# Performance work log

Hardware: AMD Instinct MI355X
Metric: run time of the kernel (lower is better)

## Reference

```python
import jax, jax.numpy as jnp
import numpy as np

B, S, D = 4, 2048, 1024
R = 64
N_FQK = N_FV = N_RQK = N_RV = 32
N_HEADS = 16
D_HEAD = D // N_HEADS


def setup_inputs() -> dict:
    key = jax.random.key(0)
    ks = jax.random.split(key, 10)

    def orth_bank(k, n, rows, cols):
        # mimic per-slice orthogonal init
        a = jax.random.normal(k, (n, rows, cols), dtype=jnp.float32)
        q, _ = jnp.linalg.qr(a) if rows >= cols else (jnp.swapaxes(jnp.linalg.qr(jnp.swapaxes(a, -1, -2))[0], -1, -2), None)
        return q.astype(jnp.float32)

    return {
        "x": jax.random.normal(ks[0], (B, S, D), dtype=jnp.float32),
        "fqk_weights": jax.random.uniform(ks[1], (B, S, N_FQK), dtype=jnp.float32),
        "fv_weights": jax.random.uniform(ks[2], (B, S, N_FV), dtype=jnp.float32),
        "rqk_weights_Q": jax.random.uniform(ks[3], (B, S, N_RQK), dtype=jnp.float32),
        "rqk_weights_K": jax.random.uniform(ks[4], (B, S, N_RQK), dtype=jnp.float32),
        "rv_weights": jax.random.uniform(ks[5], (B, S, N_RV), dtype=jnp.float32),
        "f_neurons": orth_bank(ks[6], N_FQK + N_FV, D, R),   # (64, D, R)
        "r_neurons": orth_bank(ks[7], N_RQK + N_RV, R, D),   # (64, R, D)
        "W_O": jax.random.normal(ks[8], (D, D), dtype=jnp.float32) * (1.0 / np.sqrt(D)),
    }


def reference(x, fqk_weights, fv_weights, rqk_weights_Q, rqk_weights_K, rv_weights,
              f_neurons, r_neurons, W_O):
    fqk = f_neurons[:N_FQK]          # (N, D, R)
    fv = f_neurons[N_FQK:]
    rqk = r_neurons[:N_RQK]          # (N, R, D)
    rv = r_neurons[N_RQK:]

    # Fused routed low-rank projections (same math as bsn,ndr->bsdr then bsd,bsdr->bsr,
    # reassociated to avoid the (B,S,D,R) intermediate).
    h_qk = jnp.einsum('bsd,bsn,ndr->bsr', x, fqk_weights, fqk)
    h_v = jnp.einsum('bsd,bsn,ndr->bsr', x, fv_weights, fv)

    Q = jnp.einsum('bsr,bsn,nrd->bsd', h_qk, rqk_weights_Q, rqk)
    K = jnp.einsum('bsr,bsn,nrd->bsd', h_qk, rqk_weights_K, rqk)
    V = jnp.einsum('bsr,bsn,nrd->bsd', h_v, rv_weights, rv)

    def heads(t):  # (B,S,D) -> (B,H,S,Dh)
        return t.reshape(B, S, N_HEADS, D_HEAD).transpose(0, 2, 1, 3)

    Qh, Kh, Vh = heads(Q), heads(K), heads(V)
    scores = jnp.einsum('bhqd,bhkd->bhqk', Qh, Kh) / np.sqrt(D_HEAD).astype(np.float32)
    causal = jnp.triu(jnp.ones((S, S), dtype=bool), k=1)
    scores = jnp.where(causal[None, None], -jnp.inf, scores)
    attn = jax.nn.softmax(scores, axis=-1)
    attn_out = jnp.einsum('bhqk,bhkd->bhqd', attn, Vh)
    attn_out = attn_out.transpose(0, 2, 1, 3).reshape(B, S, D)
    return attn_out @ W_O.T
```

## Files before the change

### kernel.cpp

```cpp
#include <hip/hip_runtime.h>
#include <hip/hip_bf16.h>


namespace {
constexpr int kS = 2048;
constexpr int kD = 1024;
}

typedef unsigned short u16;
typedef __attribute__((ext_vector_type(4))) float f32x4;
typedef __attribute__((ext_vector_type(8))) short s8v;

union FragU { s8v s; unsigned u[4]; };

__device__ __forceinline__ u16 f2bf_bits(float f) {
  union { float f; unsigned u; } cv; cv.f = f;
  unsigned u = cv.u;
  unsigned r = u + 0x7fffu + ((u >> 16) & 1u);
  return (u16)(r >> 16);
}
__device__ __forceinline__ float bf2f(u16 b) {
  union { unsigned u; float f; } cv; cv.u = ((unsigned)b) << 16; return cv.f;
}
__device__ __forceinline__ unsigned pk_bf16(float a, float b) {
  __hip_bfloat162 h = __float22bfloat162_rn(make_float2(a, b));
  union { __hip_bfloat162 h; unsigned u; } cv; cv.h = h; return cv.u;
}

__global__ __launch_bounds__(256) void t1_kernel(const float* __restrict__ f,
                                                 u16* __restrict__ FT) {
  __shared__ float Tt[64 * 132];
  const int tid = threadIdx.x;
  const int d0 = blockIdx.x * 128;
  const int n  = blockIdx.y;
#pragma unroll
  for (int e = 0; e < 8; ++e) {
    int flat = tid + e * 256;
    int dd = flat >> 4, r4 = (flat & 15) * 4;
    float4 v = *(const float4*)&f[((size_t)n * kD + d0 + dd) * 64 + r4];
    Tt[(r4 + 0) * 132 + dd] = v.x;
    Tt[(r4 + 1) * 132 + dd] = v.y;
    Tt[(r4 + 2) * 132 + dd] = v.z;
    Tt[(r4 + 3) * 132 + dd] = v.w;
  }
  __syncthreads();
#pragma unroll
  for (int e = 0; e < 4; ++e) {
    int flat = tid + e * 256;
    int r = flat >> 4, dq = (flat & 15) * 8;
    const float* p = &Tt[r * 132 + dq];
    uint4 o = { pk_bf16(p[0], p[1]), pk_bf16(p[2], p[3]),
                pk_bf16(p[4], p[5]), pk_bf16(p[6], p[7]) };
    *(uint4*)&FT[((size_t)n * 64 + r) * kD + d0 + dq] = o;
  }
}

__global__ __launch_bounds__(256) void t2_kernel(const float* __restrict__ rn,
                                                 u16* __restrict__ RT) {
  __shared__ float Tt[128 * 68];
  const int tid = threadIdx.x;
  const int d0 = blockIdx.x * 128;
  const int n  = blockIdx.y;
#pragma unroll
  for (int e = 0; e < 8; ++e) {
    int flat = tid + e * 256;
    int r = flat >> 5, d4 = (flat & 31) * 4;
    float4 v = *(const float4*)&rn[((size_t)n * 64 + r) * kD + d0 + d4];
    Tt[(d4 + 0) * 68 + r] = v.x;
    Tt[(d4 + 1) * 68 + r] = v.y;
    Tt[(d4 + 2) * 68 + r] = v.z;
    Tt[(d4 + 3) * 68 + r] = v.w;
  }
  __syncthreads();
#pragma unroll
  for (int e = 0; e < 4; ++e) {
    int flat = tid + e * 256;
    int dd = flat >> 3, rq = (flat & 7) * 8;
    const float* p = &Tt[dd * 68 + rq];
    uint4 o = { pk_bf16(p[0], p[1]), pk_bf16(p[2], p[3]),
                pk_bf16(p[4], p[5]), pk_bf16(p[6], p[7]) };
    *(uint4*)&RT[((size_t)(d0 + dd)) * 4096 + n * 64 + rq] = o;
  }
}

__global__ __launch_bounds__(256) void g_gemm(const float* __restrict__ x,
                                              const u16* __restrict__ FT,
                                              u16* __restrict__ G) {
  __shared__ short As[128 * 72];
  __shared__ short Bs[128 * 72];
  const int tid = threadIdx.x;
  const int lane = tid & 63, wid = tid >> 6;
  const int wm = wid & 1, wn = wid >> 1;
  const int quad = lane >> 4, l15 = lane & 15;
  const int cT = blockIdx.x * 128;
  const int tok0 = blockIdx.y * 128;

  f32x4 acc[4][4];
#pragma unroll
  for (int mt = 0; mt < 4; ++mt)
#pragma unroll
    for (int nt = 0; nt < 4; ++nt) acc[mt][nt] = {0.f, 0.f, 0.f, 0.f};

#pragma unroll 1
  for (int d0 = 0; d0 < kD; d0 += 64) {
    __syncthreads();
#pragma unroll
    for (int e = 0; e < 8; ++e) {
      int flat = tid + e * 256;
      int row = flat >> 4, kq = (flat & 15) * 4;
      float4 v = *(const float4*)&x[(size_t)(tok0 + row) * kD + d0 + kq];
      uint2 o = { pk_bf16(v.x, v.y), pk_bf16(v.z, v.w) };
      *(uint2*)&As[row * 72 + kq] = o;
    }
#pragma unroll
    for (int e = 0; e < 4; ++e) {
      int flat = tid + e * 256;
      int col = flat >> 3, kq = (flat & 7) * 8;
      *(s8v*)&Bs[col * 72 + kq] =
          *(const s8v*)&FT[(size_t)(cT + col) * kD + d0 + kq];
    }
    __syncthreads();
    s8v a0[4], a1[4], b0[4], b1[4];
#pragma unroll
    for (int mt = 0; mt < 4; ++mt) {
      const short* p = &As[(wm * 64 + mt * 16 + l15) * 72 + quad * 8];
      a0[mt] = *(const s8v*)p;
      a1[mt] = *(const s8v*)(p + 32);
    }
#pragma unroll
    for (int nt = 0; nt < 4; ++nt) {
      const short* p = &Bs[(wn * 64 + nt * 16 + l15) * 72 + quad * 8];
      b0[nt] = *(const s8v*)p;
      b1[nt] = *(const s8v*)(p + 32);
    }
#pragma unroll
    for (int mt = 0; mt < 4; ++mt)
#pragma unroll
      for (int nt = 0; nt < 4; ++nt) {
        acc[mt][nt] = __builtin_amdgcn_mfma_f32_16x16x32_bf16(
            a0[mt], b0[nt], acc[mt][nt], 0, 0, 0);
        acc[mt][nt] = __builtin_amdgcn_mfma_f32_16x16x32_bf16(
            a1[mt], b1[nt], acc[mt][nt], 0, 0, 0);
      }
  }
#pragma unroll
  for (int mt = 0; mt < 4; ++mt)
#pragma unroll
    for (int nt = 0; nt < 4; ++nt) {
      int col = cT + wn * 64 + nt * 16 + l15;
      int rbase = tok0 + wm * 64 + mt * 16 + quad * 4;
#pragma unroll
      for (int i = 0; i < 4; ++i)
        G[(size_t)(rbase + i) * 4096 + col] = f2bf_bits(acc[mt][nt][i]);
    }
}

__global__ __launch_bounds__(256) void reduce_h(const u16* __restrict__ G,
                                                const float* __restrict__ fqk_w,
                                                const float* __restrict__ fv_w,
                                                float* __restrict__ h_qk,
                                                float* __restrict__ h_v) {
  int idx = blockIdx.x * 256 + threadIdx.x;
  int t = idx >> 4, r4 = (idx & 15) * 4;
  float4 aq = {0.f, 0.f, 0.f, 0.f}, av = {0.f, 0.f, 0.f, 0.f};
  const u16* gq = &G[(size_t)t * 4096 + r4];
  const u16* gv = gq + 2048;
#pragma unroll 4
  for (int n = 0; n < 32; ++n) {
    float wa = fqk_w[t * 32 + n];
    float wb = fv_w[t * 32 + n];
    ushort4 g1 = *(const ushort4*)&gq[n * 64];
    ushort4 g2 = *(const ushort4*)&gv[n * 64];
    aq.x += wa * bf2f(g1.x); aq.y += wa * bf2f(g1.y);
    aq.z += wa * bf2f(g1.z); aq.w += wa * bf2f(g1.w);
    av.x += wb * bf2f(g2.x); av.y += wb * bf2f(g2.y);
    av.z += wb * bf2f(g2.z); av.w += wb * bf2f(g2.w);
  }
  *(float4*)&h_qk[t * 64 + r4] = aq;
  *(float4*)&h_v[t * 64 + r4] = av;
}

__global__ __launch_bounds__(256) void qkv_gemm(
    const float* __restrict__ h_qk, const float* __restrict__ h_v,
    const float* __restrict__ wq, const float* __restrict__ wk,
    const float* __restrict__ wv, const u16* __restrict__ RT,
    u16* __restrict__ Qb, u16* __restrict__ Kb, u16* __restrict__ VTg) {
  __shared__ float hs[128 * 68];
  __shared__ float wsl[128 * 33];
  short* Bs = (short*)hs;
  const int tid = threadIdx.x;
  const int lane = tid & 63, wid = tid >> 6;
  const int wm = wid & 1, wn = wid >> 1;
  const int quad = lane >> 4, l15 = lane & 15;
  const int dT = blockIdx.x * 128;
  const int tok0 = blockIdx.y * 128;
  const int which = blockIdx.z;
  const float* __restrict__ h = (which == 2) ? h_v : h_qk;
  const float* __restrict__ w = (which == 0) ? wq : (which == 1) ? wk : wv;
  const int g0 = (which == 2) ? 2048 : 0;

#pragma unroll
  for (int e = 0; e < 8; ++e) {
    int flat = tid + e * 256;
    int row = flat >> 4, rq = (flat & 15) * 4;
    *(float4*)&hs[row * 68 + rq] =
        *(const float4*)&h[(size_t)(tok0 + row) * 64 + rq];
  }
#pragma unroll
  for (int e = 0; e < 16; ++e) {
    int flat = tid + e * 256;
    int row = flat >> 5, nn = flat & 31;
    wsl[row * 33 + nn] = w[(size_t)(tok0 + row) * 32 + nn];
  }
  __syncthreads();

  f32x4 hreg[4][4];
#pragma unroll
  for (int mt = 0; mt < 4; ++mt) {
    const float* hp = &hs[(wm * 64 + mt * 16 + l15) * 68 + quad * 8];
    hreg[mt][0] = *(const f32x4*)hp;
    hreg[mt][1] = *(const f32x4*)(hp + 4);
    hreg[mt][2] = *(const f32x4*)(hp + 32);
    hreg[mt][3] = *(const f32x4*)(hp + 36);
  }

  f32x4 acc[4][4];
#pragma unroll
  for (int mt = 0; mt < 4; ++mt)
#pragma unroll
    for (int nt = 0; nt < 4; ++nt) acc[mt][nt] = {0.f, 0.f, 0.f, 0.f};

#pragma unroll 1
  for (int n = 0; n < 32; ++n) {
    __syncthreads();
#pragma unroll
    for (int e = 0; e < 4; ++e) {
      int flat = tid + e * 256;
      int col = flat >> 3, kq = (flat & 7) * 8;
      *(s8v*)&Bs[col * 72 + kq] =
          *(const s8v*)&RT[(size_t)(dT + col) * 4096 + g0 + n * 64 + kq];
    }
    __syncthreads();
    s8v a0[4], a1[4], b0[4], b1[4];
#pragma unroll
    for (int mt = 0; mt < 4; ++mt) {
      float wv_ = wsl[(wm * 64 + mt * 16 + l15) * 33 + n];
      FragU fa, fb;
      fa.u[0] = pk_bf16(wv_ * hreg[mt][0][0], wv_ * hreg[mt][0][1]);
      fa.u[1] = pk_bf16(wv_ * hreg[mt][0][2], wv_ * hreg[mt][0][3]);
      fa.u[2] = pk_bf16(wv_ * hreg[mt][1][0], wv_ * hreg[mt][1][1]);
      fa.u[3] = pk_bf16(wv_ * hreg[mt][1][2], wv_ * hreg[mt][1][3]);
      a0[mt] = fa.s;
      fb.u[0] = pk_bf16(wv_ * hreg[mt][2][0], wv_ * hreg[mt][2][1]);
      fb.u[1] = pk_bf16(wv_ * hreg[mt][2][2], wv_ * hreg[mt][2][3]);
      fb.u[2] = pk_bf16(wv_ * hreg[mt][3][0], wv_ * hreg[mt][3][1]);
      fb.u[3] = pk_bf16(wv_ * hreg[mt][3][2], wv_ * hreg[mt][3][3]);
      a1[mt] = fb.s;
    }
#pragma unroll
    for (int nt = 0; nt < 4; ++nt) {
      const short* p = &Bs[(wn * 64 + nt * 16 + l15) * 72 + quad * 8];
      b0[nt] = *(const s8v*)p;
      b1[nt] = *(const s8v*)(p + 32);
    }
#pragma unroll
    for (int mt = 0; mt < 4; ++mt)
#pragma unroll
      for (int nt = 0; nt < 4; ++nt) {
        acc[mt][nt] = __builtin_amdgcn_mfma_f32_16x16x32_bf16(
            a0[mt], b0[nt], acc[mt][nt], 0, 0, 0);
        acc[mt][nt] = __builtin_amdgcn_mfma_f32_16x16x32_bf16(
            a1[mt], b1[nt], acc[mt][nt], 0, 0, 0);
      }
  }

  if (which < 2) {
    u16* __restrict__ O = (which == 0) ? Qb : Kb;
#pragma unroll
    for (int mt = 0; mt < 4; ++mt)
#pragma unroll
      for (int nt = 0; nt < 4; ++nt) {
        int col = dT + wn * 64 + nt * 16 + l15;
        int rbase = tok0 + wm * 64 + mt * 16 + quad * 4;
#pragma unroll
        for (int i = 0; i < 4; ++i)
          O[(size_t)(rbase + i) * kD + col] = f2bf_bits(acc[mt][nt][i]);
      }
  } else {
#pragma unroll
    for (int mt = 0; mt < 4; ++mt)
#pragma unroll
      for (int nt = 0; nt < 4; ++nt) {
        int d = dT + wn * 64 + nt * 16 + l15;
        int hh = d >> 6, dl = d & 63;
        int t = tok0 + wm * 64 + mt * 16 + quad * 4;
        int bb = t >> 11, sl = t & 2047;
        ushort4 u = { f2bf_bits(acc[mt][nt][0]), f2bf_bits(acc[mt][nt][1]),
                      f2bf_bits(acc[mt][nt][2]), f2bf_bits(acc[mt][nt][3]) };
        *(ushort4*)&VTg[(((size_t)bb * 16 + hh) * 64 + dl) * kS + sl] = u;
      }
  }
}

__global__ __launch_bounds__(512) void attn_mfma(
    const u16* __restrict__ Qb, const u16* __restrict__ Kb,
    const u16* __restrict__ VTg, u16* __restrict__ AOb)
{
  __shared__ short Qs[128 * 72];
  __shared__ short Ks[64 * 72];
  __shared__ short VTs[64 * 72];
  __shared__ short Ps[8][16 * 72];
  const int tid = threadIdx.x;
  const int lane = tid & 63, w = tid >> 6;
  const int quad = lane >> 4, l15 = lane & 15;
  const int qb = 15 - blockIdx.x;
  const int hh = blockIdx.y, b = blockIdx.z;
  const int dh = hh * 64;
  const size_t qrow0 = (size_t)b * kS + (size_t)qb * 128;
  const int ktmax = qb * 2 + 1;
  const u16* __restrict__ vbase = VTg + ((size_t)(b * 16 + hh) * 64) * kS;

  const int prow = tid >> 3;
  const int pd8  = (tid & 7) * 8;

  *(uint4*)&Qs[prow * 72 + pd8] =
      *(const uint4*)&Qb[(qrow0 + prow) * kD + dh + pd8];
  *(uint4*)&Qs[(prow + 64) * 72 + pd8] =
      *(const uint4*)&Qb[(qrow0 + prow + 64) * kD + dh + pd8];
  *(uint4*)&Ks[prow * 72 + pd8] =
      *(const uint4*)&Kb[((size_t)b * kS + prow) * kD + dh + pd8];
  *(uint4*)&VTs[prow * 72 + pd8] =
      *(const uint4*)&vbase[(size_t)prow * kS + pd8];
  __syncthreads();

  s8v bq0 = *(const s8v*)&Qs[(w * 16 + l15) * 72 + quad * 8];
  s8v bq1 = *(const s8v*)&Qs[(w * 16 + l15) * 72 + 32 + quad * 8];

  const int q_g = qb * 128 + w * 16 + l15;
  const int qmax_w = qb * 128 + w * 16 + 15;
  float m = -INFINITY, l = 0.f;
  f32x4 O[4];
#pragma unroll
  for (int dt = 0; dt < 4; ++dt) O[dt] = {0.f, 0.f, 0.f, 0.f};

#pragma unroll 1
  for (int kt = 0; kt <= ktmax; ++kt) {
    uint4 pk, pv;
    if (kt < ktmax) {
      const size_t krn = (size_t)b * kS + (size_t)(kt + 1) * 64;
      pk = *(const uint4*)&Kb[(krn + prow) * kD + dh + pd8];
      pv = *(const uint4*)&vbase[(size_t)prow * kS + (kt + 1) * 64 + pd8];
    }

    if (kt * 64 <= qmax_w) {
      f32x4 st[4];
#pragma unroll
      for (int nt = 0; nt < 4; ++nt) {
        const short* p = &Ks[(nt * 16 + l15) * 72 + quad * 8];
        s8v ak0 = *(const s8v*)p;
        s8v ak1 = *(const s8v*)(p + 32);
        f32x4 z = {0.f, 0.f, 0.f, 0.f};
        z = __builtin_amdgcn_mfma_f32_16x16x32_bf16(ak0, bq0, z, 0, 0, 0);
        st[nt] = __builtin_amdgcn_mfma_f32_16x16x32_bf16(ak1, bq1, z, 0, 0, 0);
      }

      if (kt * 64 + 63 > qb * 128 + w * 16) {
#pragma unroll
        for (int nt = 0; nt < 4; ++nt)
#pragma unroll
          for (int i = 0; i < 4; ++i)
            if (kt * 64 + nt * 16 + quad * 4 + i > q_g) st[nt][i] = -1e30f;
      }

      float pm = -INFINITY;
#pragma unroll
      for (int nt = 0; nt < 4; ++nt)
#pragma unroll
        for (int i = 0; i < 4; ++i) pm = fmaxf(pm, st[nt][i]);
      pm = fmaxf(pm, __shfl_xor(pm, 16, 64));
      pm = fmaxf(pm, __shfl_xor(pm, 32, 64));
      float mn = fmaxf(m, pm);
      float alpha = __expf((m - mn) * 0.125f);
      m = mn;
      float p[4][4];
      float r = 0.f;
#pragma unroll
      for (int nt = 0; nt < 4; ++nt)
#pragma unroll
        for (int i = 0; i < 4; ++i) {
          p[nt][i] = __expf((st[nt][i] - mn) * 0.125f);
          r += p[nt][i];
        }
      r += __shfl_xor(r, 16, 64);
      r += __shfl_xor(r, 32, 64);
      l = l * alpha + r;
#pragma unroll
      for (int dt = 0; dt < 4; ++dt)
#pragma unroll
        for (int i = 0; i < 4; ++i) O[dt][i] *= alpha;

#pragma unroll
      for (int nt = 0; nt < 4; ++nt) {
        uint2 o = { pk_bf16(p[nt][0], p[nt][1]), pk_bf16(p[nt][2], p[nt][3]) };
        *(uint2*)&Ps[w][l15 * 72 + nt * 16 + quad * 4] = o;
      }
      s8v bp0 = *(const s8v*)&Ps[w][l15 * 72 + quad * 8];
      s8v bp1 = *(const s8v*)&Ps[w][l15 * 72 + 32 + quad * 8];
#pragma unroll
      for (int dt = 0; dt < 4; ++dt) {
        const short* p2 = &VTs[(dt * 16 + l15) * 72 + quad * 8];
        s8v av0 = *(const s8v*)p2;
        s8v av1 = *(const s8v*)(p2 + 32);
        O[dt] = __builtin_amdgcn_mfma_f32_16x16x32_bf16(av0, bp0, O[dt], 0, 0, 0);
        O[dt] = __builtin_amdgcn_mfma_f32_16x16x32_bf16(av1, bp1, O[dt], 0, 0, 0);
      }
    }

    __syncthreads();
    if (kt < ktmax) {
      *(uint4*)&Ks[prow * 72 + pd8] = pk;
      *(uint4*)&VTs[prow * 72 + pd8] = pv;
    }
    __syncthreads();
  }

  const float inv = 1.f / l;
  const size_t row = qrow0 + w * 16 + l15;
#pragma unroll
  for (int dt = 0; dt < 4; ++dt) {
    uint2 o = { pk_bf16(O[dt][0] * inv, O[dt][1] * inv),
                pk_bf16(O[dt][2] * inv, O[dt][3] * inv) };
    *(uint2*)&AOb[row * kD + dh + dt * 16 + quad * 4] = o;
  }
}

__global__ __launch_bounds__(256) void wo_gemm(const u16* __restrict__ AOb,
                                               const float* __restrict__ WO,
                                               float* __restrict__ out) {
  __shared__ short As[128 * 72];
  __shared__ short Bs[128 * 72];
  const int tid = threadIdx.x;
  const int lane = tid & 63, wid = tid >> 6;
  const int wm = wid & 1, wn = wid >> 1;
  const int quad = lane >> 4, l15 = lane & 15;
  const int dT = blockIdx.x * 128;
  const int tok0 = blockIdx.y * 128;

  f32x4 acc[4][4];
#pragma unroll
  for (int mt = 0; mt < 4; ++mt)
#pragma unroll
    for (int nt = 0; nt < 4; ++nt) acc[mt][nt] = {0.f, 0.f, 0.f, 0.f};

#pragma unroll 1
  for (int e0 = 0; e0 < kD; e0 += 64) {
    __syncthreads();
#pragma unroll
    for (int e = 0; e < 4; ++e) {
      int flat = tid + e * 256;
      int row = flat >> 3, kq = (flat & 7) * 8;
      *(s8v*)&As[row * 72 + kq] =
          *(const s8v*)&AOb[(size_t)(tok0 + row) * kD + e0 + kq];
    }
#pragma unroll
    for (int e = 0; e < 8; ++e) {
      int flat = tid + e * 256;
      int col = flat >> 4, kq = (flat & 15) * 4;
      float4 v = *(const float4*)&WO[(size_t)(dT + col) * kD + e0 + kq];
      uint2 o = { pk_bf16(v.x, v.y), pk_bf16(v.z, v.w) };
      *(uint2*)&Bs[col * 72 + kq] = o;
    }
    __syncthreads();
    s8v a0[4], a1[4], b0[4], b1[4];
#pragma unroll
    for (int mt = 0; mt < 4; ++mt) {
      const short* p = &As[(wm * 64 + mt * 16 + l15) * 72 + quad * 8];
      a0[mt] = *(const s8v*)p;
      a1[mt] = *(const s8v*)(p + 32);
    }
#pragma unroll
    for (int nt = 0; nt < 4; ++nt) {
      const short* p = &Bs[(wn * 64 + nt * 16 + l15) * 72 + quad * 8];
      b0[nt] = *(const s8v*)p;
      b1[nt] = *(const s8v*)(p + 32);
    }
#pragma unroll
    for (int mt = 0; mt < 4; ++mt)
#pragma unroll
      for (int nt = 0; nt < 4; ++nt) {
        acc[mt][nt] = __builtin_amdgcn_mfma_f32_16x16x32_bf16(
            a0[mt], b0[nt], acc[mt][nt], 0, 0, 0);
        acc[mt][nt] = __builtin_amdgcn_mfma_f32_16x16x32_bf16(
            a1[mt], b1[nt], acc[mt][nt], 0, 0, 0);
      }
  }
#pragma unroll
  for (int mt = 0; mt < 4; ++mt)
#pragma unroll
    for (int nt = 0; nt < 4; ++nt) {
      int col = dT + wn * 64 + nt * 16 + l15;
      int rbase = tok0 + wm * 64 + mt * 16 + quad * 4;
#pragma unroll
      for (int i = 0; i < 4; ++i)
        out[(size_t)(rbase + i) * kD + col] = acc[mt][nt][i];
    }
}

extern "C" void kernel_launch(void* const* d_in, const int* in_sizes, int n_in,
                              void* d_out, int out_size, void* d_ws, size_t ws_size,
                              hipStream_t stream) {
  const float* x     = (const float*)d_in[0];
  const float* fqk_w = (const float*)d_in[1];
  const float* fv_w  = (const float*)d_in[2];
  const float* wq    = (const float*)d_in[3];
  const float* wk    = (const float*)d_in[4];
  const float* wv    = (const float*)d_in[5];
  const float* f_neu = (const float*)d_in[6];
  const float* r_neu = (const float*)d_in[7];
  const float* WO    = (const float*)d_in[8];
  float* out = (float*)d_out;

  char* ws = (char*)d_ws;
  u16*   FT   = (u16*)  (ws);
  u16*   RT   = (u16*)  (ws + ((size_t)8u  << 20));
  u16*   G    = (u16*)  (ws + ((size_t)16u << 20));
  float* h_qk = (float*)(ws + ((size_t)80u << 20));
  float* h_v  = (float*)(ws + ((size_t)82u << 20));
  u16*   Qb   = (u16*)  (ws + ((size_t)16u << 20));
  u16*   Kb   = (u16*)  (ws + ((size_t)32u << 20));
  u16*   VTg  = (u16*)  (ws + ((size_t)48u << 20));
  u16*   AOb  = (u16*)  (ws + ((size_t)64u << 20));

  hipLaunchKernelGGL(t1_kernel, dim3(8, 64), dim3(256), 0, stream, f_neu, FT);
  hipLaunchKernelGGL(t2_kernel, dim3(8, 64), dim3(256), 0, stream, r_neu, RT);
  hipLaunchKernelGGL(g_gemm, dim3(32, 64), dim3(256), 0, stream, x, FT, G);
  hipLaunchKernelGGL(reduce_h, dim3(512), dim3(256), 0, stream,
                     G, fqk_w, fv_w, h_qk, h_v);
  hipLaunchKernelGGL(qkv_gemm, dim3(8, 64, 3), dim3(256), 0, stream,
                     h_qk, h_v, wq, wk, wv, RT, Qb, Kb, VTg);
  hipLaunchKernelGGL(attn_mfma, dim3(16, 16, 4), dim3(512), 0, stream,
                     Qb, Kb, VTg, AOb);
  hipLaunchKernelGGL(wo_gemm, dim3(8, 64), dim3(256), 0, stream,
                     AOb, WO, out);
}
```

Baseline: 545.0 us.

## Pre-convert x and W_O to bf16 and stage GEMM tiles via direct global-to-LDS loads

Adds small conversion kernels that turn x and W_O into bf16 once, so the GEMMs no longer convert fp32 inside every tile load and read half the bytes. The g_gemm, qkv_gemm and wo_gemm tile loads now use global_load_lds to copy 16-byte chunks straight into LDS. The LDS layout changes from a padded stride to an XOR-swizzled unpadded one to avoid bank conflicts. This costs two extra launches and an extra pass over x, and wob reuses the RT workspace region after qkv_gemm has finished with it.

```diff
diff --git a/kernel.cpp b/kernel.cpp
--- a/kernel.cpp
+++ b/kernel.cpp
@@ -25,6 +25,21 @@
 __device__ __forceinline__ unsigned pk_bf16(float a, float b) {
   __hip_bfloat162 h = __float22bfloat162_rn(make_float2(a, b));
   union { __hip_bfloat162 h; unsigned u; } cv; cv.h = h; return cv.u;
+}
+__device__ __forceinline__ void gl_lds16(const void* g, void* l) {
+  __builtin_amdgcn_global_load_lds(
+      (const __attribute__((address_space(1))) unsigned int*)g,
+      (__attribute__((address_space(3))) unsigned int*)l, 16, 0, 0);
+}
+
+__global__ __launch_bounds__(256) void conv_x(const float* __restrict__ x,
+                                              u16* __restrict__ xb) {
+  int idx = blockIdx.x * 256 + threadIdx.x;
+  float4 v0 = ((const float4*)x)[idx * 2];
+  float4 v1 = ((const float4*)x)[idx * 2 + 1];
+  uint4 o = { pk_bf16(v0.x, v0.y), pk_bf16(v0.z, v0.w),
+              pk_bf16(v1.x, v1.y), pk_bf16(v1.z, v1.w) };
+  ((uint4*)xb)[idx] = o;
 }
 
 __global__ __launch_bounds__(256) void t1_kernel(const float* __restrict__ f,
@@ -83,11 +98,11 @@
   }
 }
 
-__global__ __launch_bounds__(256) void g_gemm(const float* __restrict__ x,
+__global__ __launch_bounds__(256) void g_gemm(const u16* __restrict__ xb,
                                               const u16* __restrict__ FT,
                                               u16* __restrict__ G) {
-  __shared__ short As[128 * 72];
-  __shared__ short Bs[128 * 72];
+  __shared__ short As[128 * 64];
+  __shared__ short Bs[128 * 64];
   const int tid = threadIdx.x;
   const int lane = tid & 63, wid = tid >> 6;
   const int wm = wid & 1, wn = wid >> 1;
@@ -105,33 +120,30 @@
   for (int d0 = 0; d0 < kD; d0 += 64) {
     __syncthreads();
 #pragma unroll
-    for (int e = 0; e < 8; ++e) {
-      int flat = tid + e * 256;
-      int row = flat >> 4, kq = (flat & 15) * 4;
-      float4 v = *(const float4*)&x[(size_t)(tok0 + row) * kD + d0 + kq];
-      uint2 o = { pk_bf16(v.x, v.y), pk_bf16(v.z, v.w) };
-      *(uint2*)&As[row * 72 + kq] = o;
-    }
-#pragma unroll
     for (int e = 0; e < 4; ++e) {
       int flat = tid + e * 256;
-      int col = flat >> 3, kq = (flat & 7) * 8;
-      *(s8v*)&Bs[col * 72 + kq] =
-          *(const s8v*)&FT[(size_t)(cT + col) * kD + d0 + kq];
+      int r = flat >> 3, u = (flat & 7) ^ (r & 7);
+      gl_lds16(&xb[(size_t)(tok0 + r) * kD + d0 + u * 8], &As[flat * 8]);
+    }
+#pragma unroll
+    for (int e = 0; e < 4; ++e) {
+      int flat = tid + e * 256;
+      int r = flat >> 3, u = (flat & 7) ^ (r & 7);
+      gl_lds16(&FT[(size_t)(cT + r) * kD + d0 + u * 8], &Bs[flat * 8]);
     }
     __syncthreads();
     s8v a0[4], a1[4], b0[4], b1[4];
 #pragma unroll
     for (int mt = 0; mt < 4; ++mt) {
-      const short* p = &As[(wm * 64 + mt * 16 + l15) * 72 + quad * 8];
-      a0[mt] = *(const s8v*)p;
-      a1[mt] = *(const s8v*)(p + 32);
+      int r = wm * 64 + mt * 16 + l15;
+      a0[mt] = *(const s8v*)&As[r * 64 + ((quad) ^ (r & 7)) * 8];
+      a1[mt] = *(const s8v*)&As[r * 64 + ((4 + quad) ^ (r & 7)) * 8];
     }
 #pragma unroll
     for (int nt = 0; nt < 4; ++nt) {
-      const short* p = &Bs[(wn * 64 + nt * 16 + l15) * 72 + quad * 8];
-      b0[nt] = *(const s8v*)p;
-      b1[nt] = *(const s8v*)(p + 32);
+      int r = wn * 64 + nt * 16 + l15;
+      b0[nt] = *(const s8v*)&Bs[r * 64 + ((quad) ^ (r & 7)) * 8];
+      b1[nt] = *(const s8v*)&Bs[r * 64 + ((4 + quad) ^ (r & 7)) * 8];
     }
 #pragma unroll
     for (int mt = 0; mt < 4; ++mt)
@@ -236,9 +248,9 @@
 #pragma unroll
     for (int e = 0; e < 4; ++e) {
       int flat = tid + e * 256;
-      int col = flat >> 3, kq = (flat & 7) * 8;
-      *(s8v*)&Bs[col * 72 + kq] =
-          *(const s8v*)&RT[(size_t)(dT + col) * 4096 + g0 + n * 64 + kq];
+      int r = flat >> 3, u = (flat & 7) ^ (r & 7);
+      gl_lds16(&RT[(size_t)(dT + r) * 4096 + g0 + n * 64 + u * 8],
+               &Bs[flat * 8]);
     }
     __syncthreads();
     s8v a0[4], a1[4], b0[4], b1[4];
@@ -259,9 +271,9 @@
     }
 #pragma unroll
     for (int nt = 0; nt < 4; ++nt) {
-      const short* p = &Bs[(wn * 64 + nt * 16 + l15) * 72 + quad * 8];
-      b0[nt] = *(const s8v*)p;
-      b1[nt] = *(const s8v*)(p + 32);
+      int r = wn * 64 + nt * 16 + l15;
+      b0[nt] = *(const s8v*)&Bs[r * 64 + ((quad) ^ (r & 7)) * 8];
+      b1[nt] = *(const s8v*)&Bs[r * 64 + ((4 + quad) ^ (r & 7)) * 8];
     }
 #pragma unroll
     for (int mt = 0; mt < 4; ++mt)
@@ -300,6 +312,16 @@
         *(ushort4*)&VTg[(((size_t)bb * 16 + hh) * 64 + dl) * kS + sl] = u;
       }
   }
+}
+
+__global__ __launch_bounds__(256) void conv_wo(const float* __restrict__ WO,
+                                               u16* __restrict__ wob) {
+  int idx = blockIdx.x * 256 + threadIdx.x;
+  float4 v0 = ((const float4*)WO)[idx * 2];
+  float4 v1 = ((const float4*)WO)[idx * 2 + 1];
+  uint4 o = { pk_bf16(v0.x, v0.y), pk_bf16(v0.z, v0.w),
+              pk_bf16(v1.x, v1.y), pk_bf16(v1.z, v1.w) };
+  ((uint4*)wob)[idx] = o;
 }
 
 __global__ __launch_bounds__(512) void attn_mfma(
@@ -435,10 +457,10 @@
 }
 
 __global__ __launch_bounds__(256) void wo_gemm(const u16* __restrict__ AOb,
-                                               const float* __restrict__ WO,
+                                               const u16* __restrict__ wob,
                                                float* __restrict__ out) {
-  __shared__ short As[128 * 72];
-  __shared__ short Bs[128 * 72];
+  __shared__ short As[128 * 64];
+  __shared__ short Bs[128 * 64];
   const int tid = threadIdx.x;
   const int lane = tid & 63, wid = tid >> 6;
   const int wm = wid & 1, wn = wid >> 1;
@@ -458,31 +480,28 @@
 #pragma unroll
     for (int e = 0; e < 4; ++e) {
       int flat = tid + e * 256;
-      int row = flat >> 3, kq = (flat & 7) * 8;
-      *(s8v*)&As[row * 72 + kq] =
-          *(const s8v*)&AOb[(size_t)(tok0 + row) * kD + e0 + kq];
-    }
-#pragma unroll
-    for (int e = 0; e < 8; ++e) {
+      int r = flat >> 3, u = (flat & 7) ^ (r & 7);
+      gl_lds16(&AOb[(size_t)(tok0 + r) * kD + e0 + u * 8], &As[flat * 8]);
+    }
+#pragma unroll
+    for (int e = 0; e < 4; ++e) {
       int flat = tid + e * 256;
-      int col = flat >> 4, kq = (flat & 15) * 4;
-      float4 v = *(const float4*)&WO[(size_t)(dT + col) * kD + e0 + kq];
-      uint2 o = { pk_bf16(v.x, v.y), pk_bf16(v.z, v.w) };
-      *(uint2*)&Bs[col * 72 + kq] = o;
+      int r = flat >> 3, u = (flat & 7) ^ (r & 7);
+      gl_lds16(&wob[(size_t)(dT + r) * kD + e0 + u * 8], &Bs[flat * 8]);
     }
     __syncthreads();
     s8v a0[4], a1[4], b0[4], b1[4];
 #pragma unroll
     for (int mt = 0; mt < 4; ++mt) {
-      const short* p = &As[(wm * 64 + mt * 16 + l15) * 72 + quad * 8];
-      a0[mt] = *(const s8v*)p;
-      a1[mt] = *(const s8v*)(p + 32);
+      int r = wm * 64 + mt * 16 + l15;
+      a0[mt] = *(const s8v*)&As[r * 64 + ((quad) ^ (r & 7)) * 8];
+      a1[mt] = *(const s8v*)&As[r * 64 + ((4 + quad) ^ (r & 7)) * 8];
     }
 #pragma unroll
     for (int nt = 0; nt < 4; ++nt) {
-      const short* p = &Bs[(wn * 64 + nt * 16 + l15) * 72 + quad * 8];
-      b0[nt] = *(const s8v*)p;
-      b1[nt] = *(const s8v*)(p + 32);
+      int r = wn * 64 + nt * 16 + l15;
+      b0[nt] = *(const s8v*)&Bs[r * 64 + ((quad) ^ (r & 7)) * 8];
+      b1[nt] = *(const s8v*)&Bs[r * 64 + ((4 + quad) ^ (r & 7)) * 8];
     }
 #pragma unroll
     for (int mt = 0; mt < 4; ++mt)
@@ -523,6 +542,7 @@
   char* ws = (char*)d_ws;
   u16*   FT   = (u16*)  (ws);
   u16*   RT   = (u16*)  (ws + ((size_t)8u  << 20));
+  u16*   wob  = (u16*)  (ws + ((size_t)8u  << 20));
   u16*   G    = (u16*)  (ws + ((size_t)16u << 20));
   float* h_qk = (float*)(ws + ((size_t)80u << 20));
   float* h_v  = (float*)(ws + ((size_t)82u << 20));
@@ -530,16 +550,19 @@
   u16*   Kb   = (u16*)  (ws + ((size_t)32u << 20));
   u16*   VTg  = (u16*)  (ws + ((size_t)48u << 20));
   u16*   AOb  = (u16*)  (ws + ((size_t)64u << 20));
-
+  u16*   xb   = (u16*)  (ws + ((size_t)84u << 20));
+
+  hipLaunchKernelGGL(conv_x, dim3(4096), dim3(256), 0, stream, x, xb);
   hipLaunchKernelGGL(t1_kernel, dim3(8, 64), dim3(256), 0, stream, f_neu, FT);
   hipLaunchKernelGGL(t2_kernel, dim3(8, 64), dim3(256), 0, stream, r_neu, RT);
-  hipLaunchKernelGGL(g_gemm, dim3(32, 64), dim3(256), 0, stream, x, FT, G);
+  hipLaunchKernelGGL(g_gemm, dim3(32, 64), dim3(256), 0, stream, xb, FT, G);
   hipLaunchKernelGGL(reduce_h, dim3(512), dim3(256), 0, stream,
                      G, fqk_w, fv_w, h_qk, h_v);
   hipLaunchKernelGGL(qkv_gemm, dim3(8, 64, 3), dim3(256), 0, stream,
                      h_qk, h_v, wq, wk, wv, RT, Qb, Kb, VTg);
+  hipLaunchKernelGGL(conv_wo, dim3(512), dim3(256), 0, stream, WO, wob);
   hipLaunchKernelGGL(attn_mfma, dim3(16, 16, 4), dim3(512), 0, stream,
                      Qb, Kb, VTg, AOb);
   hipLaunchKernelGGL(wo_gemm, dim3(8, 64), dim3(256), 0, stream,
-                     AOb, WO, out);
-}
+                     AOb, wob, out);
+}
```

Result: faster. 493.6 us (-9.4%).
